# Optimization experiments

Hardware: AMD Instinct MI355X
Metric: run time of the kernel (lower is better)

## Reference

```python
import jax, jax.numpy as jnp
import numpy as np

B, T, IN, H, OUT = 16384, 60, 1, 50, 1


def setup_inputs() -> dict:
    key = jax.random.key(0)
    ks = jax.random.split(key, 7)
    s = 1.0 / np.sqrt(H)
    return {
        "input_seq": jax.random.normal(ks[0], (B, T, IN), dtype=jnp.float32),
        "w_ih": jax.random.uniform(ks[1], (4 * H, IN), jnp.float32, -s, s),
        "w_hh": jax.random.uniform(ks[2], (4 * H, H), jnp.float32, -s, s),
        "b_ih": jax.random.uniform(ks[3], (4 * H,), jnp.float32, -s, s),
        "b_hh": jax.random.uniform(ks[4], (4 * H,), jnp.float32, -s, s),
        "w_lin": jax.random.uniform(ks[5], (OUT, H * T), jnp.float32, -s, s),
        "b_lin": jax.random.uniform(ks[6], (OUT,), jnp.float32, -s, s),
    }


def reference(input_seq, w_ih, w_hh, b_ih, b_hh, w_lin, b_lin):
    # Precompute input projections for all timesteps: [T, B, 4H]
    x_proj = jnp.einsum('bti,gi->tbg', input_seq, w_ih) + b_ih + b_hh

    def step(carry, xp):
        h, c = carry
        gates = xp + h @ w_hh.T  # [B, 4H]
        i, f, g, o = jnp.split(gates, 4, axis=-1)  # PyTorch gate order
        i, f, o = jax.nn.sigmoid(i), jax.nn.sigmoid(f), jax.nn.sigmoid(o)
        g = jnp.tanh(g)
        c = f * c + i * g
        h = o * jnp.tanh(c)
        return (h, c), h

    h0 = jnp.zeros((input_seq.shape[0], H), dtype=input_seq.dtype)
    (_, _), hs = jax.lax.scan(step, (h0, h0), x_proj)  # hs: [T, B, H]
    lstm_out = jnp.transpose(hs, (1, 0, 2)).reshape(-1, H * T)  # [B, T*H]
    return lstm_out @ w_lin.T + b_lin
```

## Files before the change

### kernel.cpp

```cpp
#include <hip/hip_runtime.h>


namespace {
constexpr int TS = 60;

typedef _Float16 half8 __attribute__((ext_vector_type(8)));
typedef _Float16 half2v __attribute__((ext_vector_type(2)));
typedef float f32x4 __attribute__((ext_vector_type(4)));
typedef float f32x2 __attribute__((ext_vector_type(2)));

__device__ __forceinline__ float fexp2(float x) { return __builtin_amdgcn_exp2f(x); }
__device__ __forceinline__ float frcp(float x) { return __builtin_amdgcn_rcpf(x); }
__device__ __forceinline__ f32x4 mfma16(half8 a, half8 b, f32x4 c) {
  return __builtin_amdgcn_mfma_f32_16x16x32_f16(a, b, c, 0, 0, 0);
}
}

__global__ __launch_bounds__(512, 4) void lstm_w8x2(
    const float* __restrict__ x,
    const float* __restrict__ w_ih,
    const float* __restrict__ w_hh,
    const float* __restrict__ b_ih,
    const float* __restrict__ b_hh,
    const float* __restrict__ w_lin,
    const float* __restrict__ b_lin,
    float* __restrict__ out)
{
  __shared__ unsigned Hs[2][2][512];
  __shared__ float WL[TS * 64];
  __shared__ float XL[TS * 32];
  __shared__ float OB[8][2][16];

  const int tid = threadIdx.x;
  const int lane = tid & 63;
  const int wv = tid >> 6;
  const int g = lane >> 4;
  const int cl = lane & 15;
  const int s8 = cl & 7;
  const long bbase = (long)blockIdx.x * 32;

  for (int i = tid; i < TS * 32; i += 512) {
    const int b = i / TS, t = i - b * TS;
    XL[t * 32 + b] = x[bbase * TS + i];
  }
  for (int i = tid; i < TS * 64; i += 512) {
    const int t = i >> 6, u = i & 63;
    WL[i] = (u < 50) ? w_lin[t * 50 + u] : 0.0f;
  }
  for (int i = tid; i < 2048; i += 512) ((unsigned*)Hs)[i] = 0u;

  half8 A[2][2];
  {
    const int gate = cl & 3, ur = cl >> 2;
#pragma unroll
    for (int tau = 0; tau < 2; ++tau) {
      const int T = 2 * wv + tau;
      const int uA = 16 * ur + T;
      const int orig = gate * 50 + uA;
      const bool valid = (uA < 50);
#pragma unroll
      for (int kc = 0; kc < 2; ++kc) {
        half8 frag;
#pragma unroll
        for (int e = 0; e < 8; ++e) {
          const int k = kc * 32 + 8 * g + e;
          float v = 0.0f;
          if (valid) {
            if (k < 50) v = w_hh[orig * 50 + k];
            else if (k == 62) v = b_ih[orig] + b_hh[orig];
            else if (k == 63) v = w_ih[orig];
          }
          frag[e] = (_Float16)v;
        }
        A[tau][kc] = frag;
      }
    }
  }
  __syncthreads();

  if (wv == 7 && g == 3) {
#pragma unroll
    for (int grp = 0; grp < 2; ++grp) {
      const half2v sp = {(_Float16)1.0f, (_Float16)XL[grp * 16 + cl]};
      Hs[grp][0][cl * 32 + (((7 ^ s8) << 2) | 3)] =
          __builtin_bit_cast(unsigned, sp);
    }
  }
  __syncthreads();

  const int rowdw = cl * 32;
  const int rd0 = rowdw + ((g ^ s8) << 2);
  const int rd1 = rowdw + (((4 | g) ^ s8) << 2);
  const int hw = 16 * g + 2 * wv;
  const int wd = rowdw + ((((hw >> 3) ^ s8) << 2) | ((hw & 7) >> 1));

  float c[2][2] = {{0.f, 0.f}, {0.f, 0.f}};
  float oacc[2] = {0.f, 0.f};

  constexpr float L1 = 1.4426950408889634f;
  constexpr float L2 = 2.8853900817779268f;

#pragma unroll 1
  for (int t = 0; t < TS; ++t) {
    const int p = t & 1;
    half8 B0[2], B1[2];
#pragma unroll
    for (int grp = 0; grp < 2; ++grp) {
      B0[grp] = *(const half8*)&Hs[grp][p][rd0];
      B1[grp] = *(const half8*)&Hs[grp][p][rd1];
    }
    f32x4 d[2][2];
#pragma unroll
    for (int grp = 0; grp < 2; ++grp) {
#pragma unroll
      for (int tau = 0; tau < 2; ++tau) {
        f32x4 a = {0.f, 0.f, 0.f, 0.f};
        a = mfma16(A[tau][0], B0[grp], a);
        a = mfma16(A[tau][1], B1[grp], a);
        d[grp][tau] = a;
      }
    }
    const f32x2 wl = *(const f32x2*)&WL[t * 64 + hw];

    half2v hh[2];
#pragma unroll
    for (int grp = 0; grp < 2; ++grp) {
#pragma unroll
      for (int tau = 0; tau < 2; ++tau) {
        const float E1 = fexp2(-L1 * d[grp][tau][0]);
        const float E2 = fexp2(-L1 * d[grp][tau][1]);
        const float E3 = fexp2(-L1 * d[grp][tau][3]);
        const float E4 = fexp2(L2 * d[grp][tau][2]);
        const float P1 = 1.0f + E1, P2 = 1.0f + E2;
        const float P3 = 1.0f + E3, P4 = 1.0f + E4;
        const float p12 = P1 * P2, p34 = P3 * P4;
        const float r = frcp(p12 * p34);
        const float r12 = r * p34, r34 = r * p12;
        const float si = r12 * P2, sf = r12 * P1;
        const float so = r34 * P4;
        const float tg = fmaf(-2.0f, r34 * P3, 1.0f);
        const float cn = fmaf(sf, c[grp][tau], si * tg);
        c[grp][tau] = cn;
        const float Ec = fexp2(L2 * cn);
        const float tc = fmaf(-2.0f, frcp(1.0f + Ec), 1.0f);
        const float hn = so * tc;
        oacc[grp] = fmaf(hn, wl[tau], oacc[grp]);
        hh[grp][tau] = (_Float16)hn;
      }
    }

    if (wv == 7 && g == 3) {
      const int tn = (t + 1 < TS) ? (t + 1) : (TS - 1);
      hh[0][0] = (_Float16)1.0f;
      hh[0][1] = (_Float16)XL[tn * 32 + cl];
      hh[1][0] = (_Float16)1.0f;
      hh[1][1] = (_Float16)XL[tn * 32 + 16 + cl];
    }
    Hs[0][p ^ 1][wd] = __builtin_bit_cast(unsigned, hh[0]);
    Hs[1][p ^ 1][wd] = __builtin_bit_cast(unsigned, hh[1]);
    __syncthreads();
  }

  oacc[0] += __shfl_xor(oacc[0], 32);
  oacc[0] += __shfl_xor(oacc[0], 16);
  oacc[1] += __shfl_xor(oacc[1], 32);
  oacc[1] += __shfl_xor(oacc[1], 16);
  if (lane < 16) {
    OB[wv][0][cl] = oacc[0];
    OB[wv][1][cl] = oacc[1];
  }
  __syncthreads();
  if (tid < 32) {
    const int grp = tid >> 4, b = tid & 15;
    float s = b_lin[0];
#pragma unroll
    for (int q = 0; q < 8; ++q) s += OB[q][grp][b];
    out[bbase + grp * 16 + b] = s;
  }
}

extern "C" void kernel_launch(void* const* d_in, const int* in_sizes, int n_in,
                              void* d_out, int out_size, void* d_ws, size_t ws_size,
                              hipStream_t stream) {
  const float* x     = (const float*)d_in[0];
  const float* w_ih  = (const float*)d_in[1];
  const float* w_hh  = (const float*)d_in[2];
  const float* b_ih  = (const float*)d_in[3];
  const float* b_hh  = (const float*)d_in[4];
  const float* w_lin = (const float*)d_in[5];
  const float* b_lin = (const float*)d_in[6];
  float* out = (float*)d_out;

  dim3 grid(16384 / 32);
  dim3 block(512);
  lstm_w8x2<<<grid, block, 0, stream>>>(x, w_ih, w_hh, b_ih, b_hh, w_lin,
                                        b_lin, out);
}
```

Baseline: 99.78 us.

## Repack LSTM gate tiles into 13 tiles across 4 waves per block

Changes the unit-to-tile mapping so the 50 hidden units are covered by 13 MFMA tiles instead of 16, removing padded tile work. Blocks shrink to 4 waves, with three waves handling 4 tiles each and one wave handling a single tile plus the input/bias column. The hidden-state buffer switches to per-element fp16 stores. Each wave now carries a longer serial chain per timestep and the work is unbalanced across waves, which may raise per-step latency at low occupancy.

Result: faster. 91.35 us (-8.4%).

```diff
diff --git a/kernel.cpp b/kernel.cpp
--- a/kernel.cpp
+++ b/kernel.cpp
@@ -7,7 +7,6 @@
 typedef _Float16 half8 __attribute__((ext_vector_type(8)));
 typedef _Float16 half2v __attribute__((ext_vector_type(2)));
 typedef float f32x4 __attribute__((ext_vector_type(4)));
-typedef float f32x2 __attribute__((ext_vector_type(2)));
 
 __device__ __forceinline__ float fexp2(float x) { return __builtin_amdgcn_exp2f(x); }
 __device__ __forceinline__ float frcp(float x) { return __builtin_amdgcn_rcpf(x); }
@@ -16,7 +15,7 @@
 }
 }
 
-__global__ __launch_bounds__(512, 4) void lstm_w8x2(
+__global__ __launch_bounds__(256, 2) void lstm_t13(
     const float* __restrict__ x,
     const float* __restrict__ w_ih,
     const float* __restrict__ w_hh,
@@ -26,10 +25,10 @@
     const float* __restrict__ b_lin,
     float* __restrict__ out)
 {
-  __shared__ unsigned Hs[2][2][512];
+  __shared__ __align__(16) _Float16 Hs[2][2][16 * 64];
   __shared__ float WL[TS * 64];
   __shared__ float XL[TS * 32];
-  __shared__ float OB[8][2][16];
+  __shared__ float OB[4][2][16];
 
   const int tid = threadIdx.x;
   const int lane = tid & 63;
@@ -39,28 +38,29 @@
   const int s8 = cl & 7;
   const long bbase = (long)blockIdx.x * 32;
 
-  for (int i = tid; i < TS * 32; i += 512) {
+  for (int i = tid; i < TS * 32; i += 256) {
     const int b = i / TS, t = i - b * TS;
     XL[t * 32 + b] = x[bbase * TS + i];
   }
-  for (int i = tid; i < TS * 64; i += 512) {
+  for (int i = tid; i < TS * 64; i += 256) {
     const int t = i >> 6, u = i & 63;
     WL[i] = (u < 50) ? w_lin[t * 50 + u] : 0.0f;
   }
-  for (int i = tid; i < 2048; i += 512) ((unsigned*)Hs)[i] = 0u;
-
-  half8 A[2][2];
+  for (int i = tid; i < 2048; i += 256) ((unsigned*)Hs)[i] = 0u;
+
+  half8 A[4][2];
   {
-    const int gate = cl & 3, ur = cl >> 2;
-#pragma unroll
-    for (int tau = 0; tau < 2; ++tau) {
-      const int T = 2 * wv + tau;
-      const int uA = 16 * ur + T;
+    const int gate = cl & 3, du = cl >> 2;
+    const int ntile = (wv < 3) ? 4 : 1;
+#pragma unroll
+    for (int tau = 0; tau < 4; ++tau) {
+      const int T = (wv < 3) ? (4 * wv + tau) : 12;
+      const int uA = 4 * T + du;
       const int orig = gate * 50 + uA;
-      const bool valid = (uA < 50);
+      const bool valid = (tau < ntile) && (uA < 50);
 #pragma unroll
       for (int kc = 0; kc < 2; ++kc) {
-        half8 frag;
+        half8 fr;
 #pragma unroll
         for (int e = 0; e < 8; ++e) {
           const int k = kc * 32 + 8 * g + e;
@@ -70,96 +70,98 @@
             else if (k == 62) v = b_ih[orig] + b_hh[orig];
             else if (k == 63) v = w_ih[orig];
           }
-          frag[e] = (_Float16)v;
+          fr[e] = (_Float16)v;
         }
-        A[tau][kc] = frag;
+        A[tau][kc] = fr;
       }
     }
   }
   __syncthreads();
 
-  if (wv == 7 && g == 3) {
+  if (wv == 3 && g == 3) {
 #pragma unroll
     for (int grp = 0; grp < 2; ++grp) {
       const half2v sp = {(_Float16)1.0f, (_Float16)XL[grp * 16 + cl]};
-      Hs[grp][0][cl * 32 + (((7 ^ s8) << 2) | 3)] =
-          __builtin_bit_cast(unsigned, sp);
+      *(half2v*)&Hs[grp][0][cl * 64 + ((7 ^ s8) << 3) + 6] = sp;
     }
   }
   __syncthreads();
 
-  const int rowdw = cl * 32;
-  const int rd0 = rowdw + ((g ^ s8) << 2);
-  const int rd1 = rowdw + (((4 | g) ^ s8) << 2);
-  const int hw = 16 * g + 2 * wv;
-  const int wd = rowdw + ((((hw >> 3) ^ s8) << 2) | ((hw & 7) >> 1));
-
-  float c[2][2] = {{0.f, 0.f}, {0.f, 0.f}};
+  const int rh0 = cl * 64 + ((g ^ s8) << 3);
+  const int rh1 = cl * 64 + (((4 | g) ^ s8) << 3);
+
+  float c[2][4] = {{0.f, 0.f, 0.f, 0.f}, {0.f, 0.f, 0.f, 0.f}};
   float oacc[2] = {0.f, 0.f};
 
   constexpr float L1 = 1.4426950408889634f;
   constexpr float L2 = 2.8853900817779268f;
+
+#define DO_TILES(NT, TBASE)                                                   \
+  {                                                                           \
+    f32x4 acc[2][NT];                                                         \
+    _Pragma("unroll") for (int grp = 0; grp < 2; ++grp) {                     \
+      _Pragma("unroll") for (int tau = 0; tau < NT; ++tau) {                  \
+        f32x4 a = {0.f, 0.f, 0.f, 0.f};                                       \
+        a = mfma16(A[tau][0], grp ? B0b : B0a, a);                            \
+        a = mfma16(A[tau][1], grp ? B1b : B1a, a);                            \
+        acc[grp][tau] = a;                                                    \
+      }                                                                       \
+    }                                                                         \
+    _Pragma("unroll") for (int tau = 0; tau < NT; ++tau) {                    \
+      const int u = 4 * (TBASE + tau) + g;                                    \
+      const float wlv = WL[t * 64 + u];                                       \
+      const int widx = cl * 64 + (((u >> 3) ^ s8) << 3) + (u & 7);            \
+      _Pragma("unroll") for (int grp = 0; grp < 2; ++grp) {                   \
+        const float E1 = fexp2(-L1 * acc[grp][tau][0]);                       \
+        const float E2 = fexp2(-L1 * acc[grp][tau][1]);                       \
+        const float E3 = fexp2(-L1 * acc[grp][tau][3]);                       \
+        const float E4 = fexp2(L2 * acc[grp][tau][2]);                        \
+        const float P1 = 1.0f + E1, P2 = 1.0f + E2;                           \
+        const float P3 = 1.0f + E3, P4 = 1.0f + E4;                           \
+        const float p12 = P1 * P2, p34 = P3 * P4;                             \
+        const float r = frcp(p12 * p34);                                      \
+        const float r12 = r * p34, r34 = r * p12;                             \
+        const float si = r12 * P2, sf = r12 * P1, so = r34 * P4;              \
+        const float tg = fmaf(-2.0f, r34 * P3, 1.0f);                         \
+        const float cn = fmaf(sf, c[grp][tau], si * tg);                      \
+        c[grp][tau] = cn;                                                     \
+        const float Ec = fexp2(L2 * cn);                                      \
+        const float tc = fmaf(-2.0f, frcp(1.0f + Ec), 1.0f);                  \
+        const float hn = so * tc;                                             \
+        oacc[grp] = fmaf(hn, wlv, oacc[grp]);                                 \
+        (grp ? HN1 : HN0)[widx] = (_Float16)hn;                               \
+      }                                                                       \
+    }                                                                         \
+  }
 
 #pragma unroll 1
   for (int t = 0; t < TS; ++t) {
     const int p = t & 1;
-    half8 B0[2], B1[2];
-#pragma unroll
-    for (int grp = 0; grp < 2; ++grp) {
-      B0[grp] = *(const half8*)&Hs[grp][p][rd0];
-      B1[grp] = *(const half8*)&Hs[grp][p][rd1];
-    }
-    f32x4 d[2][2];
-#pragma unroll
-    for (int grp = 0; grp < 2; ++grp) {
-#pragma unroll
-      for (int tau = 0; tau < 2; ++tau) {
-        f32x4 a = {0.f, 0.f, 0.f, 0.f};
-        a = mfma16(A[tau][0], B0[grp], a);
-        a = mfma16(A[tau][1], B1[grp], a);
-        d[grp][tau] = a;
+    const _Float16* HR0 = &Hs[0][p][0];
+    const _Float16* HR1 = &Hs[1][p][0];
+    _Float16* HN0 = &Hs[0][p ^ 1][0];
+    _Float16* HN1 = &Hs[1][p ^ 1][0];
+    const half8 B0a = *(const half8*)&HR0[rh0];
+    const half8 B1a = *(const half8*)&HR0[rh1];
+    const half8 B0b = *(const half8*)&HR1[rh0];
+    const half8 B1b = *(const half8*)&HR1[rh1];
+
+    if (wv < 3) {
+      const int tb = 4 * wv;
+      DO_TILES(4, tb);
+    } else {
+      DO_TILES(1, 12);
+      if (g == 3) {
+        const int tn = (t + 1 < TS) ? (t + 1) : (TS - 1);
+        const half2v spa = {(_Float16)1.0f, (_Float16)XL[tn * 32 + cl]};
+        const half2v spb = {(_Float16)1.0f, (_Float16)XL[tn * 32 + 16 + cl]};
+        *(half2v*)&HN0[cl * 64 + ((7 ^ s8) << 3) + 6] = spa;
+        *(half2v*)&HN1[cl * 64 + ((7 ^ s8) << 3) + 6] = spb;
       }
     }
-    const f32x2 wl = *(const f32x2*)&WL[t * 64 + hw];
-
-    half2v hh[2];
-#pragma unroll
-    for (int grp = 0; grp < 2; ++grp) {
-#pragma unroll
-      for (int tau = 0; tau < 2; ++tau) {
-        const float E1 = fexp2(-L1 * d[grp][tau][0]);
-        const float E2 = fexp2(-L1 * d[grp][tau][1]);
-        const float E3 = fexp2(-L1 * d[grp][tau][3]);
-        const float E4 = fexp2(L2 * d[grp][tau][2]);
-        const float P1 = 1.0f + E1, P2 = 1.0f + E2;
-        const float P3 = 1.0f + E3, P4 = 1.0f + E4;
-        const float p12 = P1 * P2, p34 = P3 * P4;
-        const float r = frcp(p12 * p34);
-        const float r12 = r * p34, r34 = r * p12;
-        const float si = r12 * P2, sf = r12 * P1;
-        const float so = r34 * P4;
-        const float tg = fmaf(-2.0f, r34 * P3, 1.0f);
-        const float cn = fmaf(sf, c[grp][tau], si * tg);
-        c[grp][tau] = cn;
-        const float Ec = fexp2(L2 * cn);
-        const float tc = fmaf(-2.0f, frcp(1.0f + Ec), 1.0f);
-        const float hn = so * tc;
-        oacc[grp] = fmaf(hn, wl[tau], oacc[grp]);
-        hh[grp][tau] = (_Float16)hn;
-      }
-    }
-
-    if (wv == 7 && g == 3) {
-      const int tn = (t + 1 < TS) ? (t + 1) : (TS - 1);
-      hh[0][0] = (_Float16)1.0f;
-      hh[0][1] = (_Float16)XL[tn * 32 + cl];
-      hh[1][0] = (_Float16)1.0f;
-      hh[1][1] = (_Float16)XL[tn * 32 + 16 + cl];
-    }
-    Hs[0][p ^ 1][wd] = __builtin_bit_cast(unsigned, hh[0]);
-    Hs[1][p ^ 1][wd] = __builtin_bit_cast(unsigned, hh[1]);
     __syncthreads();
   }
+#undef DO_TILES
 
   oacc[0] += __shfl_xor(oacc[0], 32);
   oacc[0] += __shfl_xor(oacc[0], 16);
@@ -174,7 +176,7 @@
     const int grp = tid >> 4, b = tid & 15;
     float s = b_lin[0];
 #pragma unroll
-    for (int q = 0; q < 8; ++q) s += OB[q][grp][b];
+    for (int q = 0; q < 4; ++q) s += OB[q][grp][b];
     out[bbase + grp * 16 + b] = s;
   }
 }
@@ -192,7 +194,7 @@
   float* out = (float*)d_out;
 
   dim3 grid(16384 / 32);
-  dim3 block(512);
-  lstm_w8x2<<<grid, block, 0, stream>>>(x, w_ih, w_hh, b_ih, b_hh, w_lin,
-                                        b_lin, out);
-}
+  dim3 block(256);
+  lstm_t13<<<grid, block, 0, stream>>>(x, w_ih, w_hh, b_ih, b_hh, w_lin,
+                                       b_lin, out);
+}
```
